# Performance work log

Measured on AMD Instinct MI355X. Metric: run time of the kernel, lower is better.

The kernel has to match this reference:

```python
import jax, jax.numpy as jnp
import numpy as np


def _haar_dwt(x):
    # pywt 'haar' dwt2 on even-sized inputs: non-overlapping 2x2 blocks.
    # For block [[a,b],[c,d]]: cA=(a+b+c+d)/2, cH=(a+b-c-d)/2,
    # cV=(a-b+c-d)/2, cD=(a-b-c+d)/2  (pywt dec_hi = [-1/sqrt2, 1/sqrt2]).
    B, C, H, W = x.shape
    xb = x.reshape(B, C, H // 2, 2, W // 2, 2)
    a = xb[:, :, :, 0, :, 0]
    b = xb[:, :, :, 0, :, 1]
    c = xb[:, :, :, 1, :, 0]
    d = xb[:, :, :, 1, :, 1]
    ll = (a + b + c + d) * 0.5
    ch = (a + b - c - d) * 0.5
    cv = (a - b + c - d) * 0.5
    cd = (a - b - c + d) * 0.5
    return ll, ch, cv, cd


def _haar_idwt(ll, ch, cv, cd):
    a = (ll + ch + cv + cd) * 0.5
    b = (ll + ch - cv - cd) * 0.5
    c = (ll - ch + cv - cd) * 0.5
    d = (ll - ch - cv + cd) * 0.5
    B, C, h2, w2 = ll.shape
    top = jnp.stack([a, b], axis=-1)   # [B,C,h2,w2,2]
    bot = jnp.stack([c, d], axis=-1)   # [B,C,h2,w2,2]
    y = jnp.stack([top, bot], axis=-3)  # [B,C,h2,2,w2,2]
    return y.reshape(B, C, 2 * h2, 2 * w2)


def _conv2d(x, w, b, groups=1, pad=1):
    y = jax.lax.conv_general_dilated(
        x, w, window_strides=(1, 1), padding=[(pad, pad), (pad, pad)],
        dimension_numbers=('NCHW', 'OIHW', 'NCHW'), feature_group_count=groups)
    return y + b[None, :, None, None]


def setup_inputs() -> dict:
    key = jax.random.key(0)
    ks = jax.random.split(key, 7)
    B, C, H, W = 8, 64, 256, 256
    C4 = 4 * C
    x = jax.random.normal(ks[0], (B, C, H, W), dtype=jnp.float32)
    dw_w = jax.random.normal(ks[1], (C4, 1, 3, 3), dtype=jnp.float32) / 3.0
    dw_b = jax.random.normal(ks[2], (C4,), dtype=jnp.float32) * 0.01
    pw_w = jax.random.normal(ks[3], (C4, C4, 1, 1), dtype=jnp.float32) / float(np.sqrt(C4))
    pw_b = jax.random.normal(ks[4], (C4,), dtype=jnp.float32) * 0.01
    cv_w = jax.random.normal(ks[5], (C4, C4, 3, 3), dtype=jnp.float32) / float(3.0 * np.sqrt(C4))
    cv_b = jax.random.normal(ks[6], (C4,), dtype=jnp.float32) * 0.01
    return {"x": x, "dw_w": dw_w, "dw_b": dw_b, "pw_w": pw_w,
            "pw_b": pw_b, "cv_w": cv_w, "cv_b": cv_b}


def reference(x, dw_w, dw_b, pw_w, pw_b, cv_w, cv_b):
    B, C, H, W = x.shape  # source math requires H == W (spatial transpose)
    C4 = 4 * C
    ll, ch, cv, cd = _haar_dwt(x)
    # Source stores each subband spatially TRANSPOSED (transpose(2,1,0)).
    sub = jnp.stack([jnp.swapaxes(s, -1, -2) for s in (ll, ch, cv, cd)], axis=2)
    t = sub.reshape(B, C4, H // 2, W // 2)  # channel order c*4 + {LL,cH,cV,cD}
    t = _conv2d(t, dw_w, dw_b, groups=C4, pad=1)  # depthwise 3x3
    t = _conv2d(t, pw_w, pw_b, groups=1, pad=0)   # pointwise 1x1
    t = _conv2d(t, cv_w, cv_b, groups=1, pad=1)   # dense 3x3
    t = jax.nn.gelu(t, approximate=False)         # torch nn.GELU() = exact erf
    t = t.reshape(B, C, 4, H // 2, W // 2)
    # Inverse path un-transposes each subband (transpose(0,2) in source).
    ll2, ch2, cv2, cd2 = [jnp.swapaxes(t[:, :, k], -1, -2) for k in range(4)]
    return _haar_idwt(ll2, ch2, cv2, cd2)
```

## Files before the change

### kernel.cpp

```cpp
#include <hip/hip_runtime.h>
#include <hip/hip_bf16.h>

#define DEVI __device__ __forceinline__

typedef __attribute__((ext_vector_type(8))) short abf8;
typedef __attribute__((ext_vector_type(4))) float f32x4;

DEVI unsigned short f2bf(float f) {
  union { __hip_bfloat16 h; unsigned short u; } cvt;
  cvt.h = __float2bfloat16(f);
  return cvt.u;
}
DEVI float bf2f(unsigned short u) {
  return __uint_as_float(((unsigned)u) << 16);
}
DEVI void async16(const void* g, void* l) {
  __builtin_amdgcn_global_load_lds((__attribute__((address_space(1))) void*)(g),
                                   (__attribute__((address_space(3))) void*)(l), 16, 0, 0);
}

__global__ __launch_bounds__(256) void k0w(const float* __restrict__ cv_w,
                                           const float* __restrict__ pw_w,
                                           const float* __restrict__ pw_b,
                                           unsigned short* __restrict__ cvb,
                                           float* __restrict__ pb3) {
  __shared__ __align__(16) unsigned short As[128 * 32];
  __shared__ __align__(16) unsigned short Bs[128 * 32];
  const int t = threadIdx.x;
  const int wv = t >> 6, ln = t & 63, q = ln >> 4, cl = ln & 15;
  const int dd = blockIdx.x;
  const int oc0 = blockIdx.y * 128, ic0 = blockIdx.z * 128;
  f32x4 acc[2][8] = {};
  float pacc = 0.0f;
  for (int m0 = 0; m0 < 256; m0 += 32) {
    __syncthreads();
    {
      const int ocr = t >> 1, h = t & 1;
      const float* src = cv_w + ((size_t)(oc0 + ocr) * 256 + m0 + h * 16) * 9 + dd;
      unsigned short* dstp = As + ocr * 32 + h * 16;
      for (int j = 0; j < 16; ++j) dstp[j] = f2bf(src[j * 9]);
    }
    for (int idx = t; idx < 4096; idx += 256) {
      int r = idx >> 7, c = idx & 127;
      Bs[c * 32 + r] = f2bf(pw_w[(size_t)(m0 + r) * 256 + ic0 + c]);
    }
    __syncthreads();
    if (blockIdx.z == 0 && t < 128) {
      for (int mk = 0; mk < 32; ++mk) pacc += bf2f(As[t * 32 + mk]) * pw_b[m0 + mk];
    }
    abf8 a0 = *(const abf8*)(As + (wv * 32 + cl) * 32 + q * 8);
    abf8 a1 = *(const abf8*)(As + (wv * 32 + 16 + cl) * 32 + q * 8);
    for (int nt = 0; nt < 8; ++nt) {
      abf8 bf = *(const abf8*)(Bs + (nt * 16 + cl) * 32 + q * 8);
      acc[0][nt] = __builtin_amdgcn_mfma_f32_16x16x32_bf16(a0, bf, acc[0][nt], 0, 0, 0);
      acc[1][nt] = __builtin_amdgcn_mfma_f32_16x16x32_bf16(a1, bf, acc[1][nt], 0, 0, 0);
    }
  }
  if (blockIdx.z == 0 && t < 128) pb3[(size_t)(oc0 + t) * 9 + dd] = pacc;
  for (int mt = 0; mt < 2; ++mt)
    for (int r = 0; r < 4; ++r)
      for (int nt = 0; nt < 8; ++nt) {
        int oc = oc0 + wv * 32 + mt * 16 + q * 4 + r;
        int ic = ic0 + nt * 16 + cl;
        cvb[((size_t)dd << 16) + oc * 256 + ic] = f2bf(acc[mt][nt][r]);
      }
}

__global__ __launch_bounds__(256) void k0q(const float* __restrict__ pb3,
                                           const float* __restrict__ cv_b,
                                           float* __restrict__ bias9) {
  const int oc = threadIdx.x;
  float p[9];
  for (int i = 0; i < 9; ++i) p[i] = pb3[oc * 9 + i];
  const float cb = cv_b[oc];
  for (int uc = 0; uc < 3; ++uc)
    for (int vc = 0; vc < 3; ++vc) {
      int du0 = (uc == 0) ? 1 : 0, du1 = (uc == 2) ? 1 : 2;
      int dv0 = (vc == 0) ? 1 : 0, dv1 = (vc == 2) ? 1 : 2;
      float s = cb;
      for (int du = du0; du <= du1; ++du)
        for (int dv = dv0; dv <= dv1; ++dv) s += p[du * 3 + dv];
      bias9[(uc * 3 + vc) * 256 + oc] = s;
    }
}

__global__ __launch_bounds__(256) void k1a_dwt(const float* __restrict__ x,
                                               unsigned short* __restrict__ t0) {
  __shared__ __align__(16) float L[64 * 65];
  const int t = threadIdx.x;
  const int u0 = (blockIdx.x & 3) * 32;
  const int v0 = (blockIdx.x >> 2) * 32;
  const int c = blockIdx.y, b = blockIdx.z;
  const float* xp = x + (((size_t)(b * 64 + c)) << 16);
  {
    const int row = t >> 2;
    const float* xr = xp + (size_t)(2 * v0 + row) * 256 + 2 * u0;
    float* Lr = L + row * 65;
    for (int j = 0; j < 4; ++j) {
      int col = ((t & 3) + j * 4) * 4;
      float4 val = *(const float4*)(xr + col);
      Lr[col] = val.x; Lr[col + 1] = val.y; Lr[col + 2] = val.z; Lr[col + 3] = val.w;
    }
  }
  __syncthreads();
  const int vv = t & 31;
  const int us = t >> 5;
  const size_t outc = ((size_t)(b * 256 + c * 4)) << 14;
  for (int pass = 0; pass < 4; ++pass) {
    int uu = us * 4 + pass;
    const float* Lp = L + (2 * vv) * 65 + 2 * uu;
    float a = Lp[0], bb = Lp[1], cc = Lp[65], dd = Lp[66];
    float sll = (a + bb + cc + dd) * 0.5f;
    float sch = (a + bb - cc - dd) * 0.5f;
    float scv = (a - bb + cc - dd) * 0.5f;
    float scd = (a - bb - cc + dd) * 0.5f;
    size_t base = outc + ((u0 + uu) << 7) + (v0 + vv);
    t0[base]         = f2bf(sll);
    t0[base + 16384] = f2bf(sch);
    t0[base + 32768] = f2bf(scv);
    t0[base + 49152] = f2bf(scd);
  }
}

__global__ __launch_bounds__(256) void k1b_dw(const unsigned short* __restrict__ t0,
                                              const float* __restrict__ dww,
                                              const float* __restrict__ dwb,
                                              unsigned short* __restrict__ t1) {
  __shared__ __align__(16) unsigned short S[32 * 181];
  __shared__ __align__(16) unsigned short O[128 * 32];
  const int t = threadIdx.x;
  const int u0 = (blockIdx.x >> 3) * 8;
  const int v0 = (blockIdx.x & 7) * 16;
  const int icB = blockIdx.y * 32;
  const int b = blockIdx.z;
  const unsigned short* t0b = t0 + (((size_t)(b * 256 + icB)) << 14);
  for (int idx = t; idx < 5760; idx += 256) {
    int ic = idx / 180;
    int r = idx - ic * 180;
    int uu = r / 18;
    int vvq = r - uu * 18;
    int gu = u0 + uu - 1, gv = v0 + vvq - 1;
    unsigned short val = 0;
    if ((unsigned)gu < 128u && (unsigned)gv < 128u)
      val = t0b[((size_t)ic << 14) + (gu << 7) + gv];
    S[ic * 181 + r] = val;
  }
  __syncthreads();
  const int icp = t & 15, uu = (t >> 4) & 7, vh = t >> 7;
  const int cc0 = icB + icp * 2;
  float w0[9], w1[9];
  const float* wp = dww + cc0 * 9;
  for (int i = 0; i < 9; ++i) { w0[i] = wp[i]; w1[i] = wp[9 + i]; }
  const float b0 = dwb[cc0], b1 = dwb[cc0 + 1];
  const unsigned short* S0 = S + (icp * 2) * 181 + uu * 18 + vh * 8;
  const unsigned short* S1 = S0 + 181;
  float a0[3][3], a1[3][3];
  for (int du = 0; du < 3; ++du)
    for (int dv = 0; dv < 2; ++dv) {
      a0[du][dv] = bf2f(S0[du * 18 + dv]);
      a1[du][dv] = bf2f(S1[du * 18 + dv]);
    }
  unsigned* O32 = (unsigned*)O;
  for (int vv = 0; vv < 8; ++vv) {
    for (int du = 0; du < 3; ++du) {
      a0[du][2] = bf2f(S0[du * 18 + vv + 2]);
      a1[du][2] = bf2f(S1[du * 18 + vv + 2]);
    }
    float s0 = b0, s1 = b1;
    for (int du = 0; du < 3; ++du)
      for (int dv = 0; dv < 3; ++dv) {
        s0 += w0[du * 3 + dv] * a0[du][dv];
        s1 += w1[du * 3 + dv] * a1[du][dv];
      }
    int p = uu * 16 + vh * 8 + vv;
    O32[p * 16 + icp] = (unsigned)f2bf(s0) | ((unsigned)f2bf(s1) << 16);
    for (int du = 0; du < 3; ++du) {
      a0[du][0] = a0[du][1]; a0[du][1] = a0[du][2];
      a1[du][0] = a1[du][1]; a1[du][1] = a1[du][2];
    }
  }
  __syncthreads();
  const int p = t >> 1, hf = t & 1;
  const int pu = p >> 4, pv = p & 15;
  size_t gp = (size_t)((u0 + pu) * 128 + (v0 + pv));
  const uint4* src = (const uint4*)(O + p * 32 + hf * 16);
  uint4* dst = (uint4*)(t1 + ((((size_t)b * 16384) + gp) << 8) + icB + hf * 16);
  dst[0] = src[0];
  dst[1] = src[1];
}

__global__ __launch_bounds__(256) void k3_cv(const unsigned short* __restrict__ t1,
                                             const unsigned short* __restrict__ cvb,
                                             const float* __restrict__ bias9,
                                             unsigned short* __restrict__ t3) {
  __shared__ __align__(16) char smem[34816];
  unsigned short* As = (unsigned short*)smem;
  unsigned short* Bs = (unsigned short*)(smem + 24576);
  unsigned short* Ost = (unsigned short*)smem;
  const int t = threadIdx.x;
  const int wv = t >> 6, ln = t & 63;
  const int oc0 = blockIdx.x * 128;
  const int u = blockIdx.y;
  const int b = blockIdx.z;
  const unsigned short* t1b = t1 + ((size_t)b << 22);
  const int q = ln >> 4, cl = ln & 15;
  const int lr = ln >> 2, sp = ln & 3;
  const int scA = (sp - (lr >> 1)) & 3;
  const int scB = (sp - ((1 + lr) >> 1)) & 3;
  const int soffA = ((q + (cl >> 1)) & 3) * 8;
  if (t < 32) ((unsigned*)Bs)[t < 16 ? t : (2064 + (t - 16))] = 0;
  f32x4 acc[2][8] = {};
  for (int du = 0; du < 3; ++du) {
    const int us = u + du - 1;
    if ((unsigned)us >= 128u) continue;
    const unsigned short* trow = t1b + ((size_t)us << 15);
    const unsigned short* wdu = cvb + (((size_t)(du * 3)) << 16);
    for (int ic0 = 0; ic0 < 256; ic0 += 32) {
      __syncthreads();
      for (int g = wv; g < 32; g += 4) {
        if (g < 24) {
          int dv = g >> 3, ch = g & 7;
          async16(wdu + (((size_t)dv) << 16) + (((size_t)(oc0 + ch * 16 + lr)) << 8) + ic0 + scA * 8,
                  As + dv * 4096 + ch * 512);
        } else {
          int ch = g - 24;
          async16(trow + (((size_t)(ch * 16 + lr)) << 8) + ic0 + scB * 8,
                  Bs + 32 + ch * 512);
        }
      }
      __syncthreads();
      for (int dv = 0; dv < 3; ++dv) {
        const unsigned short* Adv = As + dv * 4096;
        abf8 a0 = *(const abf8*)(Adv + (wv * 32 + cl) * 32 + soffA);
        abf8 a1 = *(const abf8*)(Adv + (wv * 32 + 16 + cl) * 32 + soffA);
        const int slotB = ((q + ((cl + dv) >> 1)) & 3) * 8;
        const unsigned short* Bbase = Bs + (cl + dv) * 32 + slotB;
        for (int nt = 0; nt < 8; ++nt) {
          abf8 bf = *(const abf8*)(Bbase + nt * 512);
          acc[0][nt] = __builtin_amdgcn_mfma_f32_16x16x32_bf16(a0, bf, acc[0][nt], 0, 0, 0);
          acc[1][nt] = __builtin_amdgcn_mfma_f32_16x16x32_bf16(a1, bf, acc[1][nt], 0, 0, 0);
        }
      }
    }
  }
  __syncthreads();
  const int uc = (u == 0) ? 0 : ((u == 127) ? 2 : 1);
  const float* b9 = bias9 + uc * 3 * 256;
  const bool isv0 = (cl == 0), isv127 = (cl == 15);
  for (int mt = 0; mt < 2; ++mt) {
    int ocr = wv * 32 + mt * 16 + q * 4;
    for (int r = 0; r < 4; ++r) {
      int ocA = oc0 + ocr + r;
      float bmid = b9[256 + ocA - oc0 + oc0];
      float blo  = b9[ocA];
      float bhi  = b9[512 + ocA];
      bmid = b9[256 + ocA];
      for (int nt = 0; nt < 8; ++nt) {
        float bias = bmid;
        if (nt == 0 && isv0) bias = blo;
        else if (nt == 7 && isv127) bias = bhi;
        float xv = acc[mt][nt][r] + bias;
        float u_ = 0.7978845608028654f * xv * (1.0f + 0.044715f * xv * xv);
        float e = __expf(-2.0f * fabsf(u_));
        float th = (1.0f - e) / (1.0f + e);
        th = (u_ >= 0.0f) ? th : -th;
        float g = 0.5f * xv * (1.0f + th);
        Ost[(ocr + r) * 136 + nt * 16 + cl] = f2bf(g);
      }
    }
  }
  __syncthreads();
  const int rr = t >> 1, hf = t & 1;
  const uint4* src = (const uint4*)(Ost + rr * 136 + hf * 64);
  uint4* dst = (uint4*)(t3 + ((size_t)(b * 256 + oc0 + rr) << 14) + (u << 7) + hf * 64);
  for (int j = 0; j < 8; ++j) dst[j] = src[j];
}

__global__ __launch_bounds__(256) void k4_idwt(const unsigned short* __restrict__ t3,
                                               float* __restrict__ out) {
  __shared__ __align__(16) unsigned short L[4 * 32 * 34];
  const int t = threadIdx.x;
  const int w20 = (blockIdx.x & 3) * 32;
  const int h20 = (blockIdx.x >> 2) * 32;
  const int c = blockIdx.y, b = blockIdx.z;
  const unsigned short* t3b = t3 + (((size_t)(b * 256 + c * 4)) << 14);
  {
    const int row = t >> 1, hf = t & 1;
    const int k = row >> 5, w2i = row & 31;
    const unsigned* g = (const unsigned*)(t3b + ((size_t)k << 14) + ((w20 + w2i) << 7) + h20 + hf * 16);
    unsigned* l = (unsigned*)(L + (k * 32 + w2i) * 34 + hf * 16);
    for (int j = 0; j < 8; ++j) l[j] = g[j];
  }
  __syncthreads();
  const int w2 = t & 31;
  const int h2b = t >> 5;
  float* ob = out + (((size_t)(b * 64 + c)) << 16);
  for (int pass = 0; pass < 4; ++pass) {
    int h2 = h2b + pass * 8;
    int off = w2 * 34 + h2;
    float ll = bf2f(L[off]);
    float ch = bf2f(L[off + 1088]);
    float cv = bf2f(L[off + 2176]);
    float cd = bf2f(L[off + 3264]);
    float A  = (ll + ch + cv + cd) * 0.5f;
    float Bv = (ll + ch - cv - cd) * 0.5f;
    float Cv = (ll - ch + cv - cd) * 0.5f;
    float D  = (ll - ch - cv + cd) * 0.5f;
    int hg = (h20 + h2) * 2, wg = (w20 + w2) * 2;
    *(float2*)(ob + (size_t)hg * 256 + wg)       = make_float2(A, Bv);
    *(float2*)(ob + (size_t)(hg + 1) * 256 + wg) = make_float2(Cv, D);
  }
}

extern "C" void kernel_launch(void* const* d_in, const int* in_sizes, int n_in,
                              void* d_out, int out_size, void* d_ws, size_t ws_size,
                              hipStream_t stream) {
  const float* x    = (const float*)d_in[0];
  const float* dw_w = (const float*)d_in[1];
  const float* dw_b = (const float*)d_in[2];
  const float* pw_w = (const float*)d_in[3];
  const float* pw_b = (const float*)d_in[4];
  const float* cv_w = (const float*)d_in[5];
  const float* cv_b = (const float*)d_in[6];
  char* ws = (char*)d_ws;
  float* pb3           = (float*)ws;
  float* bias9         = (float*)(ws + 16384);
  unsigned short* cvb  = (unsigned short*)(ws + 65536);
  unsigned short* bufA = (unsigned short*)(ws + (size_t)(2u << 20));
  unsigned short* bufB = (unsigned short*)(ws + (size_t)(70u << 20));
  k0w<<<dim3(9, 2, 2), 256, 0, stream>>>(cv_w, pw_w, pw_b, cvb, pb3);
  k0q<<<1, 256, 0, stream>>>(pb3, cv_b, bias9);
  k1a_dwt<<<dim3(16, 64, 8), 256, 0, stream>>>(x, bufA);
  k1b_dw<<<dim3(128, 8, 8), 256, 0, stream>>>(bufA, dw_w, dw_b, bufB);
  k3_cv<<<dim3(2, 128, 8), 256, 0, stream>>>(bufB, cvb, bias9, bufA);
  k4_idwt<<<dim3(16, 64, 8), 256, 0, stream>>>(bufA, (float*)d_out);
}
```

Measured before the change: 563.6 us.

## Compute all 256 output channels per block with three staged input rows and double-buffered taps

The dense 3x3 conv kernel now has each block compute all 256 output channels for one output row, rather than half of them. It stages the three needed input rows in LDS once per input-channel chunk and streams the nine weight taps through a double-buffered LDS region. Each input row is then loaded once instead of once per channel half, and weight loads overlap the MFMA work. The cost is twice the accumulator registers, more LDS (about 57KB), fewer blocks (1024) and more barriers per chunk, which may lower occupancy.

```diff
diff --git a/kernel.cpp b/kernel.cpp
--- a/kernel.cpp
+++ b/kernel.cpp
@@ -193,87 +193,103 @@
                                              const unsigned short* __restrict__ cvb,
                                              const float* __restrict__ bias9,
                                              unsigned short* __restrict__ t3) {
-  __shared__ __align__(16) char smem[34816];
+  __shared__ __align__(16) char smem[57728];
   unsigned short* As = (unsigned short*)smem;
-  unsigned short* Bs = (unsigned short*)(smem + 24576);
+  unsigned short* Bs = (unsigned short*)(smem + 32768);
   unsigned short* Ost = (unsigned short*)smem;
   const int t = threadIdx.x;
   const int wv = t >> 6, ln = t & 63;
-  const int oc0 = blockIdx.x * 128;
-  const int u = blockIdx.y;
-  const int b = blockIdx.z;
+  const int u = blockIdx.x;
+  const int b = blockIdx.y;
   const unsigned short* t1b = t1 + ((size_t)b << 22);
   const int q = ln >> 4, cl = ln & 15;
   const int lr = ln >> 2, sp = ln & 3;
   const int scA = (sp - (lr >> 1)) & 3;
   const int scB = (sp - ((1 + lr) >> 1)) & 3;
   const int soffA = ((q + (cl >> 1)) & 3) * 8;
-  if (t < 32) ((unsigned*)Bs)[t < 16 ? t : (2064 + (t - 16))] = 0;
-  f32x4 acc[2][8] = {};
-  for (int du = 0; du < 3; ++du) {
-    const int us = u + du - 1;
-    if ((unsigned)us >= 128u) continue;
-    const unsigned short* trow = t1b + ((size_t)us << 15);
-    const unsigned short* wdu = cvb + (((size_t)(du * 3)) << 16);
-    for (int ic0 = 0; ic0 < 256; ic0 += 32) {
-      __syncthreads();
-      for (int g = wv; g < 32; g += 4) {
-        if (g < 24) {
-          int dv = g >> 3, ch = g & 7;
-          async16(wdu + (((size_t)dv) << 16) + (((size_t)(oc0 + ch * 16 + lr)) << 8) + ic0 + scA * 8,
-                  As + dv * 4096 + ch * 512);
-        } else {
-          int ch = g - 24;
-          async16(trow + (((size_t)(ch * 16 + lr)) << 8) + ic0 + scB * 8,
-                  Bs + 32 + ch * 512);
-        }
-      }
-      __syncthreads();
-      for (int dv = 0; dv < 3; ++dv) {
-        const unsigned short* Adv = As + dv * 4096;
-        abf8 a0 = *(const abf8*)(Adv + (wv * 32 + cl) * 32 + soffA);
-        abf8 a1 = *(const abf8*)(Adv + (wv * 32 + 16 + cl) * 32 + soffA);
-        const int slotB = ((q + ((cl + dv) >> 1)) & 3) * 8;
-        const unsigned short* Bbase = Bs + (cl + dv) * 32 + slotB;
-        for (int nt = 0; nt < 8; ++nt) {
-          abf8 bf = *(const abf8*)(Bbase + nt * 512);
-          acc[0][nt] = __builtin_amdgcn_mfma_f32_16x16x32_bf16(a0, bf, acc[0][nt], 0, 0, 0);
-          acc[1][nt] = __builtin_amdgcn_mfma_f32_16x16x32_bf16(a1, bf, acc[1][nt], 0, 0, 0);
-        }
-      }
-    }
-  }
-  __syncthreads();
+  if (t < 96) {
+    int j = t >> 5, r = (t >> 4) & 1, w = t & 15;
+    ((unsigned*)Bs)[j * 2080 + r * 2064 + w] = 0;
+  }
+  if (u == 0)   for (int i = t; i < 2080; i += 256) ((unsigned*)Bs)[i] = 0;
+  if (u == 127) for (int i = t; i < 2080; i += 256) ((unsigned*)(Bs + 2 * 4160))[i] = 0;
+  f32x4 acc[4][8] = {};
+  for (int ic0 = 0; ic0 < 256; ic0 += 32) {
+    __syncthreads();
+    for (int g = wv; g < 24; g += 4) {
+      int j = g >> 3, ch = g & 7;
+      int us = u - 1 + j;
+      if ((unsigned)us < 128u)
+        async16(t1b + (((size_t)us) << 15) + (((size_t)(ch * 16 + lr)) << 8) + ic0 + scB * 8,
+                Bs + j * 4160 + 32 + ch * 512);
+    }
+    for (int g = wv; g < 16; g += 4)
+      async16(cvb + (((size_t)(g * 16 + lr)) << 8) + ic0 + scA * 8, As + g * 512);
+    __syncthreads();
+#pragma unroll
+    for (int tap = 0; tap < 9; ++tap) {
+      const unsigned short* Acur = As + (tap & 1) * 8192;
+      if (tap < 8) {
+        unsigned short* Anx = As + ((tap + 1) & 1) * 8192;
+        const unsigned short* wsrc = cvb + (((size_t)(tap + 1)) << 16);
+        for (int g = wv; g < 16; g += 4)
+          async16(wsrc + (((size_t)(g * 16 + lr)) << 8) + ic0 + scA * 8, Anx + g * 512);
+      }
+      const int du = tap / 3, dv = tap - (tap / 3) * 3;
+      abf8 a0 = *(const abf8*)(Acur + (wv * 64 + cl) * 32 + soffA);
+      abf8 a1 = *(const abf8*)(Acur + (wv * 64 + 16 + cl) * 32 + soffA);
+      abf8 a2 = *(const abf8*)(Acur + (wv * 64 + 32 + cl) * 32 + soffA);
+      abf8 a3 = *(const abf8*)(Acur + (wv * 64 + 48 + cl) * 32 + soffA);
+      const int slotB = ((q + ((cl + dv) >> 1)) & 3) * 8;
+      const unsigned short* Bb = Bs + du * 4160 + (cl + dv) * 32 + slotB;
+#pragma unroll
+      for (int nt = 0; nt < 8; ++nt) {
+        abf8 bf = *(const abf8*)(Bb + nt * 512);
+        acc[0][nt] = __builtin_amdgcn_mfma_f32_16x16x32_bf16(a0, bf, acc[0][nt], 0, 0, 0);
+        acc[1][nt] = __builtin_amdgcn_mfma_f32_16x16x32_bf16(a1, bf, acc[1][nt], 0, 0, 0);
+        acc[2][nt] = __builtin_amdgcn_mfma_f32_16x16x32_bf16(a2, bf, acc[2][nt], 0, 0, 0);
+        acc[3][nt] = __builtin_amdgcn_mfma_f32_16x16x32_bf16(a3, bf, acc[3][nt], 0, 0, 0);
+      }
+      if (tap < 8) __syncthreads();
+    }
+  }
   const int uc = (u == 0) ? 0 : ((u == 127) ? 2 : 1);
   const float* b9 = bias9 + uc * 3 * 256;
   const bool isv0 = (cl == 0), isv127 = (cl == 15);
-  for (int mt = 0; mt < 2; ++mt) {
-    int ocr = wv * 32 + mt * 16 + q * 4;
-    for (int r = 0; r < 4; ++r) {
-      int ocA = oc0 + ocr + r;
-      float bmid = b9[256 + ocA - oc0 + oc0];
-      float blo  = b9[ocA];
-      float bhi  = b9[512 + ocA];
-      bmid = b9[256 + ocA];
-      for (int nt = 0; nt < 8; ++nt) {
-        float bias = bmid;
-        if (nt == 0 && isv0) bias = blo;
-        else if (nt == 7 && isv127) bias = bhi;
-        float xv = acc[mt][nt][r] + bias;
-        float u_ = 0.7978845608028654f * xv * (1.0f + 0.044715f * xv * xv);
-        float e = __expf(-2.0f * fabsf(u_));
-        float th = (1.0f - e) / (1.0f + e);
-        th = (u_ >= 0.0f) ? th : -th;
-        float g = 0.5f * xv * (1.0f + th);
-        Ost[(ocr + r) * 136 + nt * 16 + cl] = f2bf(g);
-      }
-    }
-  }
-  __syncthreads();
-  const int rr = t >> 1, hf = t & 1;
-  const uint4* src = (const uint4*)(Ost + rr * 136 + hf * 64);
-  uint4* dst = (uint4*)(t3 + ((size_t)(b * 256 + oc0 + rr) << 14) + (u << 7) + hf * 64);
-  for (int j = 0; j < 8; ++j) dst[j] = src[j];
+  for (int h = 0; h < 2; ++h) {
+    __syncthreads();
+    if ((wv >> 1) == h) {
+#pragma unroll
+      for (int mt = 0; mt < 4; ++mt) {
+        int ocr = (wv & 1) * 64 + mt * 16 + q * 4;
+#pragma unroll
+        for (int r = 0; r < 4; ++r) {
+          int ocA = h * 128 + ocr + r;
+          float bmid = b9[256 + ocA];
+          float blo  = b9[ocA];
+          float bhi  = b9[512 + ocA];
+#pragma unroll
+          for (int nt = 0; nt < 8; ++nt) {
+            float bias = bmid;
+            if (nt == 0 && isv0) bias = blo;
+            else if (nt == 7 && isv127) bias = bhi;
+            float xv = acc[mt][nt][r] + bias;
+            float u_ = 0.7978845608028654f * xv * (1.0f + 0.044715f * xv * xv);
+            float e = __expf(-2.0f * fabsf(u_));
+            float th = (1.0f - e) / (1.0f + e);
+            th = (u_ >= 0.0f) ? th : -th;
+            float g = 0.5f * xv * (1.0f + th);
+            Ost[(ocr + r) * 136 + nt * 16 + cl] = f2bf(g);
+          }
+        }
+      }
+    }
+    __syncthreads();
+    const int rr = t >> 1, hf = t & 1;
+    const uint4* src = (const uint4*)(Ost + rr * 136 + hf * 64);
+    uint4* dst = (uint4*)(t3 + ((size_t)(b * 256 + h * 128 + rr) << 14) + (u << 7) + hf * 64);
+    for (int j = 0; j < 8; ++j) dst[j] = src[j];
+  }
 }
 
 __global__ __launch_bounds__(256) void k4_idwt(const unsigned short* __restrict__ t3,
@@ -332,6 +348,6 @@
   k0q<<<1, 256, 0, stream>>>(pb3, cv_b, bias9);
   k1a_dwt<<<dim3(16, 64, 8), 256, 0, stream>>>(x, bufA);
   k1b_dw<<<dim3(128, 8, 8), 256, 0, stream>>>(bufA, dw_w, dw_b, bufB);
-  k3_cv<<<dim3(2, 128, 8), 256, 0, stream>>>(bufB, cvb, bias9, bufA);
+  k3_cv<<<dim3(128, 8), 256, 0, stream>>>(bufB, cvb, bias9, bufA);
   k4_idwt<<<dim3(16, 64, 8), 256, 0, stream>>>(bufA, (float*)d_out);
 }
```

New measurement: 672.0 us. 1.19x slower.

## Double-buffer LDS staging in dense conv kernel and shrink weight-fold tiles

Applied to the files above, without the earlier changes.

The dense 3x3 conv kernel now double-buffers its A/B LDS tiles. It issues async global-to-LDS loads for the next (du, ic) step while running MFMAs on the current one, which cuts one barrier per step and flattens the loop to skip out-of-range rows. The weight-fold kernel k0w moves to 64x64 tiles over a 9x4x4 grid so more blocks run in parallel. In exchange, the conv kernel's LDS use nearly doubles to about 64KB, which can lower occupancy. There is also a possible race, because the next stage is written while other waves may still read the previous buffer only one barrier earlier.

```diff
diff --git a/kernel.cpp b/kernel.cpp
--- a/kernel.cpp
+++ b/kernel.cpp
@@ -24,46 +24,43 @@
                                            const float* __restrict__ pw_b,
                                            unsigned short* __restrict__ cvb,
                                            float* __restrict__ pb3) {
-  __shared__ __align__(16) unsigned short As[128 * 32];
-  __shared__ __align__(16) unsigned short Bs[128 * 32];
+  __shared__ __align__(16) unsigned short As[64 * 32];
+  __shared__ __align__(16) unsigned short Bs[64 * 32];
   const int t = threadIdx.x;
   const int wv = t >> 6, ln = t & 63, q = ln >> 4, cl = ln & 15;
   const int dd = blockIdx.x;
-  const int oc0 = blockIdx.y * 128, ic0 = blockIdx.z * 128;
-  f32x4 acc[2][8] = {};
+  const int oc0 = blockIdx.y * 64, ic0 = blockIdx.z * 64;
+  f32x4 acc[4] = {};
   float pacc = 0.0f;
   for (int m0 = 0; m0 < 256; m0 += 32) {
     __syncthreads();
     {
-      const int ocr = t >> 1, h = t & 1;
-      const float* src = cv_w + ((size_t)(oc0 + ocr) * 256 + m0 + h * 16) * 9 + dd;
-      unsigned short* dstp = As + ocr * 32 + h * 16;
-      for (int j = 0; j < 16; ++j) dstp[j] = f2bf(src[j * 9]);
-    }
-    for (int idx = t; idx < 4096; idx += 256) {
-      int r = idx >> 7, c = idx & 127;
+      const int ocr = t >> 2, h = t & 3;
+      const float* src = cv_w + ((size_t)(oc0 + ocr) * 256 + m0 + h * 8) * 9 + dd;
+      unsigned short* dstp = As + ocr * 32 + h * 8;
+      for (int j = 0; j < 8; ++j) dstp[j] = f2bf(src[j * 9]);
+    }
+    for (int idx = t; idx < 2048; idx += 256) {
+      int r = idx >> 6, c = idx & 63;
       Bs[c * 32 + r] = f2bf(pw_w[(size_t)(m0 + r) * 256 + ic0 + c]);
     }
     __syncthreads();
-    if (blockIdx.z == 0 && t < 128) {
+    if (blockIdx.z == 0 && t < 64) {
       for (int mk = 0; mk < 32; ++mk) pacc += bf2f(As[t * 32 + mk]) * pw_b[m0 + mk];
     }
-    abf8 a0 = *(const abf8*)(As + (wv * 32 + cl) * 32 + q * 8);
-    abf8 a1 = *(const abf8*)(As + (wv * 32 + 16 + cl) * 32 + q * 8);
-    for (int nt = 0; nt < 8; ++nt) {
+    abf8 a0 = *(const abf8*)(As + (wv * 16 + cl) * 32 + q * 8);
+    for (int nt = 0; nt < 4; ++nt) {
       abf8 bf = *(const abf8*)(Bs + (nt * 16 + cl) * 32 + q * 8);
-      acc[0][nt] = __builtin_amdgcn_mfma_f32_16x16x32_bf16(a0, bf, acc[0][nt], 0, 0, 0);
-      acc[1][nt] = __builtin_amdgcn_mfma_f32_16x16x32_bf16(a1, bf, acc[1][nt], 0, 0, 0);
-    }
-  }
-  if (blockIdx.z == 0 && t < 128) pb3[(size_t)(oc0 + t) * 9 + dd] = pacc;
-  for (int mt = 0; mt < 2; ++mt)
-    for (int r = 0; r < 4; ++r)
-      for (int nt = 0; nt < 8; ++nt) {
-        int oc = oc0 + wv * 32 + mt * 16 + q * 4 + r;
-        int ic = ic0 + nt * 16 + cl;
-        cvb[((size_t)dd << 16) + oc * 256 + ic] = f2bf(acc[mt][nt][r]);
-      }
+      acc[nt] = __builtin_amdgcn_mfma_f32_16x16x32_bf16(a0, bf, acc[nt], 0, 0, 0);
+    }
+  }
+  if (blockIdx.z == 0 && t < 64) pb3[(size_t)(oc0 + t) * 9 + dd] = pacc;
+  for (int r = 0; r < 4; ++r)
+    for (int nt = 0; nt < 4; ++nt) {
+      int oc = oc0 + wv * 16 + q * 4 + r;
+      int ic = ic0 + nt * 16 + cl;
+      cvb[((size_t)dd << 16) + oc * 256 + ic] = f2bf(acc[nt][r]);
+    }
 }
 
 __global__ __launch_bounds__(256) void k0q(const float* __restrict__ pb3,
@@ -193,9 +190,9 @@
                                              const unsigned short* __restrict__ cvb,
                                              const float* __restrict__ bias9,
                                              unsigned short* __restrict__ t3) {
-  __shared__ __align__(16) char smem[34816];
+  __shared__ __align__(16) char smem[65792];
   unsigned short* As = (unsigned short*)smem;
-  unsigned short* Bs = (unsigned short*)(smem + 24576);
+  unsigned short* Bs = (unsigned short*)(smem + 49152);
   unsigned short* Ost = (unsigned short*)smem;
   const int t = threadIdx.x;
   const int wv = t >> 6, ln = t & 63;
@@ -208,42 +205,58 @@
   const int scA = (sp - (lr >> 1)) & 3;
   const int scB = (sp - ((1 + lr) >> 1)) & 3;
   const int soffA = ((q + (cl >> 1)) & 3) * 8;
-  if (t < 32) ((unsigned*)Bs)[t < 16 ? t : (2064 + (t - 16))] = 0;
-  f32x4 acc[2][8] = {};
-  for (int du = 0; du < 3; ++du) {
+  if (t < 64) {
+    int pp = t >> 5, r = (t >> 4) & 1, w = t & 15;
+    ((unsigned*)Bs)[pp * 2080 + r * 2064 + w] = 0;
+  }
+  const int du_lo = (u == 0) ? 1 : 0;
+  const int NR = (u == 0 || u == 127) ? 16 : 24;
+
+  auto STAGE = [&](int r, int pp) {
+    const int du = du_lo + (r >> 3);
+    const int ic0 = (r & 7) << 5;
     const int us = u + du - 1;
-    if ((unsigned)us >= 128u) continue;
     const unsigned short* trow = t1b + ((size_t)us << 15);
     const unsigned short* wdu = cvb + (((size_t)(du * 3)) << 16);
-    for (int ic0 = 0; ic0 < 256; ic0 += 32) {
-      __syncthreads();
-      for (int g = wv; g < 32; g += 4) {
-        if (g < 24) {
-          int dv = g >> 3, ch = g & 7;
-          async16(wdu + (((size_t)dv) << 16) + (((size_t)(oc0 + ch * 16 + lr)) << 8) + ic0 + scA * 8,
-                  As + dv * 4096 + ch * 512);
-        } else {
-          int ch = g - 24;
-          async16(trow + (((size_t)(ch * 16 + lr)) << 8) + ic0 + scB * 8,
-                  Bs + 32 + ch * 512);
-        }
+    unsigned short* Ap = As + pp * 12288;
+    unsigned short* Bp = Bs + pp * 4160;
+    for (int g = wv; g < 32; g += 4) {
+      if (g < 24) {
+        int dv = g >> 3, ch = g & 7;
+        async16(wdu + (((size_t)dv) << 16) + (((size_t)(oc0 + ch * 16 + lr)) << 8) + ic0 + scA * 8,
+                Ap + dv * 4096 + ch * 512);
+      } else {
+        int ch = g - 24;
+        async16(trow + (((size_t)(ch * 16 + lr)) << 8) + ic0 + scB * 8,
+                Bp + 32 + ch * 512);
       }
-      __syncthreads();
-      for (int dv = 0; dv < 3; ++dv) {
-        const unsigned short* Adv = As + dv * 4096;
-        abf8 a0 = *(const abf8*)(Adv + (wv * 32 + cl) * 32 + soffA);
-        abf8 a1 = *(const abf8*)(Adv + (wv * 32 + 16 + cl) * 32 + soffA);
-        const int slotB = ((q + ((cl + dv) >> 1)) & 3) * 8;
-        const unsigned short* Bbase = Bs + (cl + dv) * 32 + slotB;
-        for (int nt = 0; nt < 8; ++nt) {
-          abf8 bf = *(const abf8*)(Bbase + nt * 512);
-          acc[0][nt] = __builtin_amdgcn_mfma_f32_16x16x32_bf16(a0, bf, acc[0][nt], 0, 0, 0);
-          acc[1][nt] = __builtin_amdgcn_mfma_f32_16x16x32_bf16(a1, bf, acc[1][nt], 0, 0, 0);
-        }
+    }
+  };
+
+  f32x4 acc[2][8] = {};
+  STAGE(0, 0);
+  __syncthreads();
+  for (int r = 0; r < NR; ++r) {
+    const int pp = r & 1;
+    if (r + 1 < NR) STAGE(r + 1, pp ^ 1);
+    const unsigned short* Ap = As + pp * 12288;
+    const unsigned short* Bp = Bs + pp * 4160;
+#pragma unroll
+    for (int dv = 0; dv < 3; ++dv) {
+      const unsigned short* Adv = Ap + dv * 4096;
+      abf8 a0 = *(const abf8*)(Adv + (wv * 32 + cl) * 32 + soffA);
+      abf8 a1 = *(const abf8*)(Adv + (wv * 32 + 16 + cl) * 32 + soffA);
+      const int slotB = ((q + ((cl + dv) >> 1)) & 3) * 8;
+      const unsigned short* Bb = Bp + (cl + dv) * 32 + slotB;
+#pragma unroll
+      for (int nt = 0; nt < 8; ++nt) {
+        abf8 bf = *(const abf8*)(Bb + nt * 512);
+        acc[0][nt] = __builtin_amdgcn_mfma_f32_16x16x32_bf16(a0, bf, acc[0][nt], 0, 0, 0);
+        acc[1][nt] = __builtin_amdgcn_mfma_f32_16x16x32_bf16(a1, bf, acc[1][nt], 0, 0, 0);
       }
     }
-  }
-  __syncthreads();
+    __syncthreads();
+  }
   const int uc = (u == 0) ? 0 : ((u == 127) ? 2 : 1);
   const float* b9 = bias9 + uc * 3 * 256;
   const bool isv0 = (cl == 0), isv127 = (cl == 15);
@@ -251,10 +264,9 @@
     int ocr = wv * 32 + mt * 16 + q * 4;
     for (int r = 0; r < 4; ++r) {
       int ocA = oc0 + ocr + r;
-      float bmid = b9[256 + ocA - oc0 + oc0];
+      float bmid = b9[256 + ocA];
       float blo  = b9[ocA];
       float bhi  = b9[512 + ocA];
-      bmid = b9[256 + ocA];
       for (int nt = 0; nt < 8; ++nt) {
         float bias = bmid;
         if (nt == 0 && isv0) bias = blo;
@@ -328,7 +340,7 @@
   unsigned short* cvb  = (unsigned short*)(ws + 65536);
   unsigned short* bufA = (unsigned short*)(ws + (size_t)(2u << 20));
   unsigned short* bufB = (unsigned short*)(ws + (size_t)(70u << 20));
-  k0w<<<dim3(9, 2, 2), 256, 0, stream>>>(cv_w, pw_w, pw_b, cvb, pb3);
+  k0w<<<dim3(9, 4, 4), 256, 0, stream>>>(cv_w, pw_w, pw_b, cvb, pb3);
   k0q<<<1, 256, 0, stream>>>(pb3, cv_b, bias9);
   k1a_dwt<<<dim3(16, 64, 8), 256, 0, stream>>>(x, bufA);
   k1b_dw<<<dim3(128, 8, 8), 256, 0, stream>>>(bufA, dw_w, dw_b, bufB);
```

New measurement: 583.2 us. 1.03x slower.
